# Kernel tuning notes

Hardware: AMD Instinct MI355X
Metric: run time of the kernel (lower is better)

The kernel has to match this reference:

```python
import jax, jax.numpy as jnp
import numpy as np

N, E, F_IN, H, K = 100000, 1600000, 256, 128, 5


def setup_inputs() -> dict:
    key = jax.random.key(0)
    ks = jax.random.split(key, 24)

    def rn(k, shape, scale=0.05):
        return jax.random.normal(k, shape, dtype=jnp.float32) * scale

    inp = {
        "x": rn(ks[0], (N, F_IN), 1.0),
        "edge_index": jax.random.randint(ks[1], (2, E), 0, N, dtype=jnp.int64),
        "edge_attr": jax.random.uniform(ks[2], (N, K), dtype=jnp.float32),
        "pre_W": rn(ks[3], (F_IN, H)),
        "pre_b": jnp.zeros((H,), jnp.float32),
        "c1_Ws": rn(ks[4], (H, H)),
        "c1_Wn": rn(ks[5], (H, H)),
        "c1_b": jnp.zeros((H,), jnp.float32),
        "c2_Ws": rn(ks[6], (H, H)),
        "c2_Wn": rn(ks[7], (H, H)),
        "c2_b": jnp.zeros((H,), jnp.float32),
        "nodepost_W": rn(ks[8], (H, H)),
        "nodepost_b": jnp.zeros((H,), jnp.float32),
        "d_W0": rn(ks[9], (K, H)),
        "d_b0": jnp.zeros((H,), jnp.float32),
        "d_W1": rn(ks[10], (H, H)),
        "d_b1": jnp.zeros((H,), jnp.float32),
        "d_W2": rn(ks[11], (H, H)),
        "d_b2": jnp.zeros((H,), jnp.float32),
        "d_W3": rn(ks[12], (H, H)),
        "d_b3": jnp.zeros((H,), jnp.float32),
        "final_W": rn(ks[13], (2 * H, 1)),
        "final_b": jnp.zeros((1,), jnp.float32),
    }
    return inp


def _mean_agg(h, src, dst, n):
    # scatter-mean of source features onto destination nodes
    s = jax.ops.segment_sum(h[src], dst, num_segments=n)  # [N, H]
    deg = jax.ops.segment_sum(jnp.ones_like(dst, dtype=h.dtype), dst, num_segments=n)
    return s / jnp.maximum(deg, 1.0)[:, None]


def reference(x, edge_index, edge_attr, pre_W, pre_b,
              c1_Ws, c1_Wn, c1_b, c2_Ws, c2_Wn, c2_b,
              nodepost_W, nodepost_b,
              d_W0, d_b0, d_W1, d_b1, d_W2, d_b2, d_W3, d_b3,
              final_W, final_b):
    n = x.shape[0]
    src, dst = edge_index[0], edge_index[1]

    # --- feat path: NodeAttributeAggregator ---
    h = x @ pre_W + pre_b                                   # pre_process_mlp
    agg = _mean_agg(h, src, dst, n)
    h = jax.nn.relu(h @ c1_Ws + agg @ c1_Wn + c1_b)          # layer1 conv + act
    agg = _mean_agg(h, src, dst, n)
    h = jax.nn.relu(h @ c2_Ws + agg @ c2_Wn + c2_b)          # layer2 conv + act
    feat_out = h @ nodepost_W + nodepost_b                   # post_process_mlp

    # --- dist path: EdgeAttributeAggregator (MLP over edge attrs) ---
    e = edge_attr.reshape(-1, K)
    y = jax.nn.relu(e @ d_W0 + d_b0)
    y = jax.nn.relu(y @ d_W1 + d_b1)
    y = jax.nn.relu(y @ d_W2 + d_b2)
    dist_out = y @ d_W3 + d_b3

    # --- merge 'cat' + final MLP + squeeze + sigmoid ---
    z = jnp.concatenate([feat_out, dist_out], axis=1)        # [N, 2H]
    out = (z @ final_W + final_b).squeeze(1)                  # [N]
    return jax.nn.sigmoid(out)
```

## Files before the change

### kernel.cpp

```cpp
#include <hip/hip_runtime.h>

#define HF 128
#define CAP 64
#define PSHIFT 17
#define BUCKET_BLOCKS 2048
#define BKS 68

typedef __attribute__((ext_vector_type(8))) short s16x8;
typedef __attribute__((ext_vector_type(4))) float f32x4;
typedef __attribute__((ext_vector_type(2))) float f32x2;

__device__ __forceinline__ unsigned short f2bf(float f) {
    unsigned u = __float_as_uint(f);
    return (unsigned short)((u + 0x7fff + ((u >> 16) & 1)) >> 16);
}

#if __has_builtin(__builtin_amdgcn_cvt_pk_fp8_f32) && __has_builtin(__builtin_amdgcn_cvt_pk_f32_fp8)
#define FP8_HW 1
#else
#define FP8_HW 0
#endif

__device__ __forceinline__ unsigned char f2fp8(float f) {
#if FP8_HW
    int v = __builtin_amdgcn_cvt_pk_fp8_f32(f, f, 0, false);
    return (unsigned char)(v & 0xff);
#else
    unsigned u = __float_as_uint(f);
    unsigned s = (u >> 24) & 0x80;
    float a = fabsf(f);
    if (a > 448.f) a = 448.f;
    if (a < 0.015625f) {
        int q = (int)(a * 512.f + 0.5f);
        return (unsigned char)(s | q);
    }
    unsigned ub = __float_as_uint(a);
    ub += 0x0007ffff + ((ub >> 20) & 1);
    int e8 = (int)(ub >> 23) - 127 + 7;
    if (e8 >= 16) return (unsigned char)(s | 0x7e);
    return (unsigned char)(s | (e8 << 3) | ((ub >> 20) & 7));
#endif
}

__device__ __forceinline__ void fp8acc4(unsigned w, float* acc) {
#if FP8_HW
    f32x2 lo = __builtin_amdgcn_cvt_pk_f32_fp8(w, false);
    f32x2 hi = __builtin_amdgcn_cvt_pk_f32_fp8(w, true);
    acc[0] += lo.x; acc[1] += lo.y; acc[2] += hi.x; acc[3] += hi.y;
#else
    #pragma unroll
    for (int j = 0; j < 4; ++j) {
        unsigned b = (w >> (8 * j)) & 0xff;
        unsigned s = (b >> 7) & 1, e = (b >> 3) & 15, m = b & 7;
        float v = e ? __uint_as_float(((e + 120) << 23) | (m << 20))
                    : (float)m * 0.001953125f;
        acc[j] += s ? -v : v;
    }
#endif
}

__device__ __forceinline__ void repack_one(
    const float* __restrict__ W, short* __restrict__ Wp, int K, int t)
{
    int nkt = K >> 5;
    int lane = t & 63;
    int kt = (t >> 6) % nkt;
    int nt = (t >> 6) / nkt;
    int c = nt * 16 + (lane & 15);
    int kbase = kt * 32 + (lane >> 4) * 8;
    s16x8 v;
    #pragma unroll
    for (int j = 0; j < 8; ++j) v[j] = (short)f2bf(W[(long)(kbase + j) * HF + c]);
    *(s16x8*)(Wp + (long)t * 8) = v;
}

__global__ __launch_bounds__(256) void repack_all(
    const float* __restrict__ preW, const float* __restrict__ c1Ws,
    const float* __restrict__ c1Wn, const float* __restrict__ c2Ws,
    const float* __restrict__ c2Wn, const float* __restrict__ dW1,
    const float* __restrict__ dW2,
    short* preWp, short* c1Wsp, short* c1Wnp, short* c2Wsp, short* c2Wnp,
    short* dW1p, short* dW2p,
    const float* __restrict__ npW, const float* __restrict__ npb,
    const float* __restrict__ dW3, const float* __restrict__ db3,
    const float* __restrict__ fW,  const float* __restrict__ fb,
    float* __restrict__ uvc)
{
    int b = blockIdx.x;
    if (b == 64) {
        int i = threadIdx.x;
        if (i < HF) {
            float u = 0.f, v = 0.f;
            for (int j = 0; j < HF; ++j) {
                u += npW[i * HF + j] * fW[j];
                v += dW3[i * HF + j] * fW[HF + j];
            }
            uvc[i] = u;
            uvc[HF + i] = v;
            if (i == 0) {
                float c = fb[0];
                for (int j = 0; j < HF; ++j) c += npb[j] * fW[j] + db3[j] * fW[HF + j];
                uvc[2 * HF] = c;
            }
        }
        return;
    }
    if (b < 16) { repack_one(preW, preWp, 256, b * 256 + threadIdx.x); return; }
    int m = (b - 16) >> 3, t = ((b - 16) & 7) * 256 + threadIdx.x;
    const float* W; short* Wp;
    switch (m) {
        case 0: W = c1Ws; Wp = c1Wsp; break;
        case 1: W = c1Wn; Wp = c1Wnp; break;
        case 2: W = c2Ws; Wp = c2Wsp; break;
        case 3: W = c2Wn; Wp = c2Wnp; break;
        case 4: W = dW1;  Wp = dW1p;  break;
        default: W = dW2; Wp = dW2p;  break;
    }
    repack_one(W, Wp, HF, t);
}

__global__ __launch_bounds__(256) void bucketx_kernel(
    const int* __restrict__ eidx, long E,
    int* __restrict__ deg, int* __restrict__ bucket, int npass)
{
    const int xcd   = blockIdx.x & 7;
    const int chunk = blockIdx.x >> 3;
    const int nchunks = BUCKET_BLOCKS / 8;
    long per = (E + nchunks - 1) / nchunks;
    per = (per + 3) & ~3L;
    const long e0 = (long)chunk * per;
    const long e1 = (e0 + per < E) ? e0 + per : E;
    if (e0 >= E) return;
    for (int p = 0; p < npass; ++p) {
        for (long e = e0 + (long)threadIdx.x * 4; e + 4 <= e1; e += 1024) {
            int4 d4 = *(const int4*)(eidx + E + e);
            #pragma unroll
            for (int j = 0; j < 4; ++j) {
                int d = (&d4.x)[j];
                if ((d >> PSHIFT) != p || ((d >> 4) & 7) != xcd) continue;
                int s = eidx[e + j];
                int pos = atomicAdd(&deg[d], 1);
                if (pos < CAP) bucket[(long)d * CAP + pos] = s;
            }
        }
        for (long e = (e1 & ~3L) + threadIdx.x; e < e1; e += 256) {
            int d = eidx[E + e];
            if ((d >> PSHIFT) != p || ((d >> 4) & 7) != xcd) continue;
            int s = eidx[e];
            int pos = atomicAdd(&deg[d], 1);
            if (pos < CAP) bucket[(long)d * CAP + pos] = s;
        }
    }
}

__device__ __forceinline__ void stage_bucket(
    const int* __restrict__ bucket, const int* __restrict__ deg,
    long row0B, int n, int* ldsbkt, int* ldsdeg)
{
    const uint4* gb = (const uint4*)(bucket + row0B * CAP);
    #pragma unroll
    for (int h = 0; h < 2; ++h) {
        int u = threadIdx.x + h * 512;
        int row = u >> 4, q = u & 15;
        *(uint4*)&ldsbkt[row * BKS + q * 4] = gb[u];
    }
    if (threadIdx.x < 64) {
        long node = row0B + threadIdx.x;
        ldsdeg[threadIdx.x] = (node < n) ? deg[node] : 0;
    }
}

__device__ __forceinline__ void agg_tile_v2(
    const unsigned char* __restrict__ hq,
    const int* ldsbkt, const int* ldsdeg,
    int n, long row0B, int wv, int lane, unsigned* ldsagg)
{
    const int r = lane >> 3;
    const int i = lane & 7;
    const int rg = wv * 8 + r;

    const int dg = ldsdeg[rg];
    const int m  = dg < CAP ? dg : CAP;
    int maxm = m;
    maxm = max(maxm, __shfl_xor(maxm, 8, 64));
    maxm = max(maxm, __shfl_xor(maxm, 16, 64));
    maxm = max(maxm, __shfl_xor(maxm, 32, 64));

    float acc[16];
    #pragma unroll
    for (int j = 0; j < 16; ++j) acc[j] = 0.f;

    const int* bl = ldsbkt + rg * BKS;
    for (int e = 0; e < maxm; e += 8) {
        int4 ia = *(const int4*)(bl + e);
        int4 ib = *(const int4*)(bl + e + 4);
        int s0 = (e + 0 < m) ? ia.x : 0;
        int s1 = (e + 1 < m) ? ia.y : 0;
        int s2 = (e + 2 < m) ? ia.z : 0;
        int s3 = (e + 3 < m) ? ia.w : 0;
        int s4 = (e + 4 < m) ? ib.x : 0;
        int s5 = (e + 5 < m) ? ib.y : 0;
        int s6 = (e + 6 < m) ? ib.z : 0;
        int s7 = (e + 7 < m) ? ib.w : 0;
        uint4 v0 = *(const uint4*)(hq + (long)s0 * HF + i * 16);
        uint4 v1 = *(const uint4*)(hq + (long)s1 * HF + i * 16);
        uint4 v2 = *(const uint4*)(hq + (long)s2 * HF + i * 16);
        uint4 v3 = *(const uint4*)(hq + (long)s3 * HF + i * 16);
        uint4 v4 = *(const uint4*)(hq + (long)s4 * HF + i * 16);
        uint4 v5 = *(const uint4*)(hq + (long)s5 * HF + i * 16);
        uint4 v6 = *(const uint4*)(hq + (long)s6 * HF + i * 16);
        uint4 v7 = *(const uint4*)(hq + (long)s7 * HF + i * 16);
        if (e + 0 < m) { fp8acc4(v0.x, acc); fp8acc4(v0.y, acc + 4); fp8acc4(v0.z, acc + 8); fp8acc4(v0.w, acc + 12); }
        if (e + 1 < m) { fp8acc4(v1.x, acc); fp8acc4(v1.y, acc + 4); fp8acc4(v1.z, acc + 8); fp8acc4(v1.w, acc + 12); }
        if (e + 2 < m) { fp8acc4(v2.x, acc); fp8acc4(v2.y, acc + 4); fp8acc4(v2.z, acc + 8); fp8acc4(v2.w, acc + 12); }
        if (e + 3 < m) { fp8acc4(v3.x, acc); fp8acc4(v3.y, acc + 4); fp8acc4(v3.z, acc + 8); fp8acc4(v3.w, acc + 12); }
        if (e + 4 < m) { fp8acc4(v4.x, acc); fp8acc4(v4.y, acc + 4); fp8acc4(v4.z, acc + 8); fp8acc4(v4.w, acc + 12); }
        if (e + 5 < m) { fp8acc4(v5.x, acc); fp8acc4(v5.y, acc + 4); fp8acc4(v5.z, acc + 8); fp8acc4(v5.w, acc + 12); }
        if (e + 6 < m) { fp8acc4(v6.x, acc); fp8acc4(v6.y, acc + 4); fp8acc4(v6.z, acc + 8); fp8acc4(v6.w, acc + 12); }
        if (e + 7 < m) { fp8acc4(v7.x, acc); fp8acc4(v7.y, acc + 4); fp8acc4(v7.z, acc + 8); fp8acc4(v7.w, acc + 12); }
    }

    const float sc = 1.f / (float)(dg > 1 ? dg : 1);
    unsigned pk[8];
    #pragma unroll
    for (int j = 0; j < 8; ++j)
        pk[j] = (unsigned)f2bf(acc[2 * j] * sc) | ((unsigned)f2bf(acc[2 * j + 1] * sc) << 16);
    const int c0 = 2 * i, c1 = 2 * i + 1, s = rg & 15;
    *(uint4*)&ldsagg[rg * 64 + ((c0 ^ s) << 2)] = make_uint4(pk[0], pk[1], pk[2], pk[3]);
    *(uint4*)&ldsagg[rg * 64 + ((c1 ^ s) << 2)] = make_uint4(pk[4], pk[5], pk[6], pk[7]);
}

__device__ __forceinline__ void gemm_pass4(
    const unsigned short* __restrict__ Av, const short* __restrict__ Wp,
    long rA, int lane, int nb, f32x4 acc[4])
{
    const int q = lane >> 4;
    #pragma unroll
    for (int kt = 0; kt < 4; ++kt) {
        s16x8 a = *(const s16x8*)(Av + rA * HF + kt * 32 + q * 8);
        #pragma unroll
        for (int j = 0; j < 4; ++j) {
            s16x8 b = *(const s16x8*)(Wp + ((long)((nb + j) * 4 + kt) * 64 + lane) * 8);
            acc[j] = __builtin_amdgcn_mfma_f32_16x16x32_bf16(a, b, acc[j], 0, 0, 0);
        }
    }
}

__device__ __forceinline__ void gemm_pass_lds4(
    const unsigned* lds, int w3, int lane, const short* __restrict__ Wp,
    int nb, f32x4 acc[4])
{
    const int q = lane >> 4;
    const int i15 = lane & 15;
    const int rl = w3 * 16 + i15;
    #pragma unroll
    for (int kt = 0; kt < 4; ++kt) {
        s16x8 a = *(const s16x8*)&lds[rl * 64 + (((kt * 4 + q) ^ i15) << 2)];
        #pragma unroll
        for (int j = 0; j < 4; ++j) {
            s16x8 b = *(const s16x8*)(Wp + ((long)((nb + j) * 4 + kt) * 64 + lane) * 8);
            acc[j] = __builtin_amdgcn_mfma_f32_16x16x32_bf16(a, b, acc[j], 0, 0, 0);
        }
    }
}

__device__ __forceinline__ void gemm_pass_mfma8(
    const unsigned short* __restrict__ Av, const short* __restrict__ Wp,
    long rA, int lane, f32x4 acc[8])
{
    const int q = lane >> 4;
    #pragma unroll
    for (int kt = 0; kt < 4; ++kt) {
        s16x8 a = *(const s16x8*)(Av + rA * HF + kt * 32 + q * 8);
        #pragma unroll
        for (int nt = 0; nt < 8; ++nt) {
            s16x8 b = *(const s16x8*)(Wp + ((long)(nt * 4 + kt) * 64 + lane) * 8);
            acc[nt] = __builtin_amdgcn_mfma_f32_16x16x32_bf16(a, b, acc[nt], 0, 0, 0);
        }
    }
}

__device__ __forceinline__ void gemm_pass_lds8(
    const unsigned* lds, int w3, int lane, const short* __restrict__ Wp, f32x4 acc[8])
{
    const int q = lane >> 4;
    const int i15 = lane & 15;
    const int rl = w3 * 16 + i15;
    #pragma unroll
    for (int kt = 0; kt < 4; ++kt) {
        s16x8 a = *(const s16x8*)&lds[rl * 64 + (((kt * 4 + q) ^ i15) << 2)];
        #pragma unroll
        for (int nt = 0; nt < 8; ++nt) {
            s16x8 b = *(const s16x8*)(Wp + ((long)(nt * 4 + kt) * 64 + lane) * 8);
            acc[nt] = __builtin_amdgcn_mfma_f32_16x16x32_bf16(a, b, acc[nt], 0, 0, 0);
        }
    }
}

__global__ __launch_bounds__(512) void prek_kernel(
    const float* __restrict__ x, const short* __restrict__ preWp,
    const float* __restrict__ preb, unsigned short* __restrict__ h0,
    unsigned char* __restrict__ h0q, int n)
{
    __shared__ float ldsx[64 * 256];
    const int lane = threadIdx.x & 63;
    const int wv   = threadIdx.x >> 6;
    const long row0B = (long)blockIdx.x * 64;

    #pragma unroll
    for (int rr = 0; rr < 8; ++rr) {
        const int row = wv * 8 + rr;
        const long gr = row0B + row;
        if (gr < n) {
            const int s = row & 7;
            const float* gp = x + gr * 256 + ((lane ^ s) << 2);
#if __has_builtin(__builtin_amdgcn_global_load_lds)
            __builtin_amdgcn_global_load_lds(
                (const __attribute__((address_space(1))) void*)gp,
                (__attribute__((address_space(3))) void*)&ldsx[row * 256], 16, 0, 0);
#else
            float4 f = *(const float4*)gp;
            *(float4*)&ldsx[row * 256 + lane * 4] = f;
#endif
        }
    }
    __syncthreads();

    const int w3 = wv & 3;
    const int nb = (wv >> 2) * 4;
    const int q  = lane >> 4;
    const int l15 = lane & 15;
    const int rl = w3 * 16 + l15;
    const int s  = rl & 7;

    f32x4 acc[4];
    #pragma unroll
    for (int j = 0; j < 4; ++j)
        #pragma unroll
        for (int i = 0; i < 4; ++i) acc[j][i] = 0.f;

    #pragma unroll
    for (int kt = 0; kt < 8; ++kt) {
        const int c0 = kt * 8 + q * 2;
        float4 f0 = *(const float4*)&ldsx[rl * 256 + ((c0 ^ s) << 2)];
        float4 f1 = *(const float4*)&ldsx[rl * 256 + (((c0 + 1) ^ s) << 2)];
        s16x8 a;
        a[0] = (short)f2bf(f0.x); a[1] = (short)f2bf(f0.y);
        a[2] = (short)f2bf(f0.z); a[3] = (short)f2bf(f0.w);
        a[4] = (short)f2bf(f1.x); a[5] = (short)f2bf(f1.y);
        a[6] = (short)f2bf(f1.z); a[7] = (short)f2bf(f1.w);
        #pragma unroll
        for (int j = 0; j < 4; ++j) {
            s16x8 b = *(const s16x8*)(preWp + ((long)((nb + j) * 8 + kt) * 64 + lane) * 8);
            acc[j] = __builtin_amdgcn_mfma_f32_16x16x32_bf16(a, b, acc[j], 0, 0, 0);
        }
    }
    __syncthreads();

    unsigned short* lp16 = (unsigned short*)ldsx;
    unsigned char*  lp8  = (unsigned char*)ldsx + 16384;
    const int cq = lane >> 4;
    #pragma unroll
    for (int j = 0; j < 4; ++j) {
        int col = (nb + j) * 16 + l15;
        float bs = preb[col];
        #pragma unroll
        for (int i = 0; i < 4; ++i) {
            int row = w3 * 16 + cq * 4 + i;
            float o = acc[j][i] + bs;
            lp16[row * 128 + col] = f2bf(o);
            lp8[row * 128 + col]  = f2fp8(o);
        }
    }
    __syncthreads();

    const int r = threadIdx.x >> 3;
    const int c = (threadIdx.x & 7) * 16;
    const long gr = row0B + r;
    if (gr < n) {
        uint4* src = (uint4*)&lp16[r * 128 + c];
        *(uint4*)(h0 + gr * HF + c)     = src[0];
        *(uint4*)(h0 + gr * HF + c + 8) = src[1];
        *(uint4*)(h0q + gr * HF + c)    = *(uint4*)&lp8[r * 128 + c];
    }
}

__global__ __launch_bounds__(512) void disthead_kernel(
    const float* __restrict__ ea, const float* __restrict__ W0,
    const float* __restrict__ b0, const short* __restrict__ W1p,
    const float* __restrict__ b1, unsigned short* __restrict__ y1, int n)
{
    __shared__ unsigned short lpk[64 * 128];
    const int lane = threadIdx.x & 63;
    const int wv   = threadIdx.x >> 6;
    const int w3   = wv & 3;
    const int nb   = (wv >> 2) * 4;
    const long row0B = (long)blockIdx.x * 64;
    const long row0 = row0B + w3 * 16;
    const int q = lane >> 4;
    long rA = row0 + (lane & 15);
    if (rA > n - 1) rA = n - 1;

    float e0 = ea[rA * 5 + 0], e1 = ea[rA * 5 + 1], e2 = ea[rA * 5 + 2],
          e3 = ea[rA * 5 + 3], e4 = ea[rA * 5 + 4];

    f32x4 acc[4];
    #pragma unroll
    for (int j = 0; j < 4; ++j)
        #pragma unroll
        for (int i = 0; i < 4; ++i) acc[j][i] = 0.f;

    #pragma unroll
    for (int kt = 0; kt < 4; ++kt) {
        const int c = kt * 32 + q * 8;
        s16x8 a;
        #pragma unroll
        for (int h = 0; h < 2; ++h) {
            float4 w0 = *(const float4*)(W0 + 0 * HF + c + h * 4);
            float4 w1 = *(const float4*)(W0 + 1 * HF + c + h * 4);
            float4 w2 = *(const float4*)(W0 + 2 * HF + c + h * 4);
            float4 w3v = *(const float4*)(W0 + 3 * HF + c + h * 4);
            float4 w4 = *(const float4*)(W0 + 4 * HF + c + h * 4);
            float4 bb = *(const float4*)(b0 + c + h * 4);
            float z0 = fmaxf(bb.x + e0 * w0.x + e1 * w1.x + e2 * w2.x + e3 * w3v.x + e4 * w4.x, 0.f);
            float z1 = fmaxf(bb.y + e0 * w0.y + e1 * w1.y + e2 * w2.y + e3 * w3v.y + e4 * w4.y, 0.f);
            float z2 = fmaxf(bb.z + e0 * w0.z + e1 * w1.z + e2 * w2.z + e3 * w3v.z + e4 * w4.z, 0.f);
            float z3 = fmaxf(bb.w + e0 * w0.w + e1 * w1.w + e2 * w2.w + e3 * w3v.w + e4 * w4.w, 0.f);
            a[h * 4 + 0] = (short)f2bf(z0); a[h * 4 + 1] = (short)f2bf(z1);
            a[h * 4 + 2] = (short)f2bf(z2); a[h * 4 + 3] = (short)f2bf(z3);
        }
        #pragma unroll
        for (int j = 0; j < 4; ++j) {
            s16x8 b = *(const s16x8*)(W1p + ((long)((nb + j) * 4 + kt) * 64 + lane) * 8);
            acc[j] = __builtin_amdgcn_mfma_f32_16x16x32_bf16(a, b, acc[j], 0, 0, 0);
        }
    }

    const int cq = lane >> 4;
    const int l15 = lane & 15;
    #pragma unroll
    for (int j = 0; j < 4; ++j) {
        int col = (nb + j) * 16 + l15;
        float bs = b1[col];
        #pragma unroll
        for (int i = 0; i < 4; ++i) {
            int row = w3 * 16 + cq * 4 + i;
            lpk[row * 128 + col] = f2bf(fmaxf(acc[j][i] + bs, 0.f));
        }
    }
    __syncthreads();

    const int r = threadIdx.x >> 3;
    const int c = (threadIdx.x & 7) * 16;
    const long gr = row0B + r;
    if (gr < n) {
        uint4* src = (uint4*)&lpk[r * 128 + c];
        *(uint4*)(y1 + gr * HF + c)     = src[0];
        *(uint4*)(y1 + gr * HF + c + 8) = src[1];
    }
}

__global__ __launch_bounds__(512) void c1f_kernel(
    const unsigned short* __restrict__ h0, const unsigned char* __restrict__ h0q,
    const int* __restrict__ deg, const int* __restrict__ bucket,
    const short* __restrict__ Wsp, const short* __restrict__ Wnp,
    const float* __restrict__ bias, unsigned short* __restrict__ out,
    unsigned char* __restrict__ outq, int n)
{
    __shared__ unsigned ldsagg[64 * 64];
    __shared__ int ldsbkt[64 * BKS];
    __shared__ int ldsdeg[64];
    const int lane = threadIdx.x & 63;
    const int wv   = threadIdx.x >> 6;
    const long row0B = (long)blockIdx.x * 64;

    stage_bucket(bucket, deg, row0B, n, ldsbkt, ldsdeg);
    __syncthreads();
    agg_tile_v2(h0q, ldsbkt, ldsdeg, n, row0B, wv, lane, ldsagg);
    __syncthreads();

    const int w3 = wv & 3;
    const int nb = (wv >> 2) * 4;

    f32x4 acc[4];
    #pragma unroll
    for (int j = 0; j < 4; ++j)
        #pragma unroll
        for (int i = 0; i < 4; ++i) acc[j][i] = 0.f;

    const long row0 = row0B + w3 * 16;
    long rA = row0 + (lane & 15);
    if (rA > n - 1) rA = n - 1;

    gemm_pass4(h0, Wsp, rA, lane, nb, acc);
    gemm_pass_lds4(ldsagg, w3, lane, Wnp, nb, acc);

    const int cq = lane >> 4;
    #pragma unroll
    for (int j = 0; j < 4; ++j) {
        int col = (nb + j) * 16 + (lane & 15);
        float bs = bias[col];
        #pragma unroll
        for (int i = 0; i < 4; ++i) {
            long r = row0 + cq * 4 + i;
            if (r < n) {
                float o = fmaxf(acc[j][i] + bs, 0.f);
                out[r * HF + col] = f2bf(o);
                outq[r * HF + col] = f2fp8(o);
            }
        }
    }
}

__global__ __launch_bounds__(512) void tailf_kernel(
    const unsigned short* __restrict__ h1, const unsigned char* __restrict__ h1q,
    const unsigned short* __restrict__ y1,
    const int* __restrict__ deg, const int* __restrict__ bucket,
    const short* __restrict__ c2Wsp, const short* __restrict__ c2Wnp,
    const short* __restrict__ dW2p,
    const float* __restrict__ c2b, const float* __restrict__ db2,
    const float* __restrict__ uvc, float* __restrict__ out, int n)
{
    __shared__ unsigned ldsagg[64 * 64];
    __shared__ int ldsbkt[64 * BKS];
    __shared__ int ldsdeg[64];
    __shared__ float pp[2][64];
    const int lane = threadIdx.x & 63;
    const int wv   = threadIdx.x >> 6;
    const long row0B = (long)blockIdx.x * 64;

    stage_bucket(bucket, deg, row0B, n, ldsbkt, ldsdeg);
    __syncthreads();
    agg_tile_v2(h1q, ldsbkt, ldsdeg, n, row0B, wv, lane, ldsagg);
    __syncthreads();

    const int w = wv & 3;
    const long row0 = row0B + w * 16;
    long rA = row0 + (lane & 15);
    if (rA > n - 1) rA = n - 1;
    const int cq = lane >> 4;
    float part[4] = {0.f, 0.f, 0.f, 0.f};

    f32x4 acc[8];
    #pragma unroll
    for (int nt = 0; nt < 8; ++nt)
        #pragma unroll
        for (int i = 0; i < 4; ++i) acc[nt][i] = 0.f;

    if (wv < 4) {
        gemm_pass_mfma8(h1, c2Wsp, rA, lane, acc);
        gemm_pass_lds8(ldsagg, w, lane, c2Wnp, acc);
        #pragma unroll
        for (int nt = 0; nt < 8; ++nt) {
            int col = nt * 16 + (lane & 15);
            float bh = c2b[col], uu = uvc[col];
            #pragma unroll
            for (int i = 0; i < 4; ++i)
                part[i] += fmaxf(acc[nt][i] + bh, 0.f) * uu;
        }
    } else {
        gemm_pass_mfma8(y1, dW2p, rA, lane, acc);
        #pragma unroll
        for (int nt = 0; nt < 8; ++nt) {
            int col = nt * 16 + (lane & 15);
            float by = db2[col], vv = uvc[HF + col];
            #pragma unroll
            for (int i = 0; i < 4; ++i)
                part[i] += fmaxf(acc[nt][i] + by, 0.f) * vv;
        }
    }

    #pragma unroll
    for (int i = 0; i < 4; ++i) {
        float s = part[i];
        s += __shfl_xor(s, 1, 64);
        s += __shfl_xor(s, 2, 64);
        s += __shfl_xor(s, 4, 64);
        s += __shfl_xor(s, 8, 64);
        part[i] = s;
    }
    if ((lane & 15) == 0) {
        #pragma unroll
        for (int i = 0; i < 4; ++i)
            pp[wv >> 2][w * 16 + cq * 4 + i] = part[i];
    }
    __syncthreads();

    if (threadIdx.x < 64) {
        long r = row0B + threadIdx.x;
        if (r < n) {
            float s = pp[0][threadIdx.x] + pp[1][threadIdx.x] + uvc[2 * HF];
            out[r] = 1.f / (1.f + expf(-s));
        }
    }
}

extern "C" void kernel_launch(void* const* d_in, const int* in_sizes, int n_in,
                              void* d_out, int out_size, void* d_ws, size_t ws_size,
                              hipStream_t stream)
{
    const float* x      = (const float*)d_in[0];
    const int*   eidx   = (const int*)  d_in[1];
    const float* eattr  = (const float*)d_in[2];
    const float* pre_W  = (const float*)d_in[3];
    const float* pre_b  = (const float*)d_in[4];
    const float* c1_Ws  = (const float*)d_in[5];
    const float* c1_Wn  = (const float*)d_in[6];
    const float* c1_b   = (const float*)d_in[7];
    const float* c2_Ws  = (const float*)d_in[8];
    const float* c2_Wn  = (const float*)d_in[9];
    const float* c2_b   = (const float*)d_in[10];
    const float* npW    = (const float*)d_in[11];
    const float* npb    = (const float*)d_in[12];
    const float* dW0    = (const float*)d_in[13];
    const float* db0    = (const float*)d_in[14];
    const float* dW1    = (const float*)d_in[15];
    const float* db1    = (const float*)d_in[16];
    const float* dW2    = (const float*)d_in[17];
    const float* db2    = (const float*)d_in[18];
    const float* dW3    = (const float*)d_in[19];
    const float* db3    = (const float*)d_in[20];
    const float* fW     = (const float*)d_in[21];
    const float* fb     = (const float*)d_in[22];

    const int  n = in_sizes[0] / 256;
    const long E = in_sizes[1] / 2;

    char* ws = (char*)d_ws;
    size_t off = 0;
    auto alloc = [&](size_t bytes) -> void* {
        void* p = ws + off;
        off += (bytes + 255) & ~(size_t)255;
        return p;
    };
    unsigned short* B0 = (unsigned short*)alloc((size_t)n * HF * 2);
    unsigned short* B1 = (unsigned short*)alloc((size_t)n * HF * 2);
    unsigned short* B2 = (unsigned short*)alloc((size_t)n * HF * 2);
    unsigned char*  B0q = (unsigned char*)alloc((size_t)n * HF);
    unsigned char*  B1q = (unsigned char*)alloc((size_t)n * HF);
    int*   deg    = (int*)alloc((size_t)n * sizeof(int));
    int*   bucket = (int*)alloc(((size_t)n + 64) * CAP * sizeof(int));
    float* uvc    = (float*)alloc((2 * HF + 1) * sizeof(float));
    short* preWp  = (short*)alloc(256 * HF * 2);
    short* c1Wsp  = (short*)alloc(HF * HF * 2);
    short* c1Wnp  = (short*)alloc(HF * HF * 2);
    short* c2Wsp  = (short*)alloc(HF * HF * 2);
    short* c2Wnp  = (short*)alloc(HF * HF * 2);
    short* dW1p   = (short*)alloc(HF * HF * 2);
    short* dW2p   = (short*)alloc(HF * HF * 2);

    const int gemmBlocks = (n + 63) / 64;
    const int npass = ((n - 1) >> PSHIFT) + 1;

    repack_all<<<65, 256, 0, stream>>>(
        pre_W, c1_Ws, c1_Wn, c2_Ws, c2_Wn, dW1, dW2,
        preWp, c1Wsp, c1Wnp, c2Wsp, c2Wnp, dW1p, dW2p,
        npW, npb, dW3, db3, fW, fb, uvc);

    hipMemsetAsync(deg, 0, (size_t)n * sizeof(int), stream);

    bucketx_kernel<<<BUCKET_BLOCKS, 256, 0, stream>>>(eidx, E, deg, bucket, npass);

    prek_kernel<<<gemmBlocks, 512, 0, stream>>>(x, preWp, pre_b, B0, B0q, n);

    disthead_kernel<<<gemmBlocks, 512, 0, stream>>>(
        eattr, dW0, db0, dW1p, db1, B2, n);

    c1f_kernel<<<gemmBlocks, 512, 0, stream>>>(
        B0, B0q, deg, bucket, c1Wsp, c1Wnp, c1_b, B1, B1q, n);

    tailf_kernel<<<gemmBlocks, 512, 0, stream>>>(
        B1, B1q, B2, deg, bucket, c2Wsp, c2Wnp, dW2p, c2_b, db2, uvc, (float*)d_out, n);
}
```

Baseline: 283.5 us.

## Replace atomic edge bucketing with a two-pass coarse-bin partition

Drops the single edge-bucketing kernel, which scanned the edge list once per XCD filter and did a global atomic per edge on the degree array. It is replaced by a two-kernel partition. The first kernel bins edges by destination range into coarse global bins, staging them in LDS and flushing in 8-entry chunks. The second kernel builds the per-node buckets and degrees for each bin using LDS atomics. The staging buffer reuses the B0 activation buffer before it is written. This adds an extra round trip of (src,dst) pairs through global memory, and edges are silently dropped if a bin overflows its capacity.

```diff
diff --git a/kernel.cpp b/kernel.cpp
--- a/kernel.cpp
+++ b/kernel.cpp
@@ -2,9 +2,9 @@
 
 #define HF 128
 #define CAP 64
-#define PSHIFT 17
-#define BUCKET_BLOCKS 2048
 #define BKS 68
+#define NBMAX 512
+#define SCAP1 8
 
 typedef __attribute__((ext_vector_type(8))) short s16x8;
 typedef __attribute__((ext_vector_type(4))) float f32x4;
@@ -119,37 +119,82 @@
     repack_one(W, Wp, HF, t);
 }
 
-__global__ __launch_bounds__(256) void bucketx_kernel(
-    const int* __restrict__ eidx, long E,
-    int* __restrict__ deg, int* __restrict__ bucket, int npass)
-{
-    const int xcd   = blockIdx.x & 7;
-    const int chunk = blockIdx.x >> 3;
-    const int nchunks = BUCKET_BLOCKS / 8;
-    long per = (E + nchunks - 1) / nchunks;
-    per = (per + 3) & ~3L;
-    const long e0 = (long)chunk * per;
+__global__ __launch_bounds__(256) void part1_kernel(
+    const int* __restrict__ eidx, long E, int nb, int sh,
+    int* __restrict__ gcount, uint2* __restrict__ binbuf, long bcap)
+{
+    __shared__ int scount[NBMAX];
+    __shared__ uint2 sbuf[NBMAX * SCAP1];
+    for (int i = threadIdx.x; i < nb; i += 256) scount[i] = 0;
+    __syncthreads();
+
+    const long per = (E + gridDim.x - 1) / gridDim.x;
+    const long e0 = (long)blockIdx.x * per;
     const long e1 = (e0 + per < E) ? e0 + per : E;
-    if (e0 >= E) return;
-    for (int p = 0; p < npass; ++p) {
-        for (long e = e0 + (long)threadIdx.x * 4; e + 4 <= e1; e += 1024) {
-            int4 d4 = *(const int4*)(eidx + E + e);
-            #pragma unroll
-            for (int j = 0; j < 4; ++j) {
-                int d = (&d4.x)[j];
-                if ((d >> PSHIFT) != p || ((d >> 4) & 7) != xcd) continue;
-                int s = eidx[e + j];
-                int pos = atomicAdd(&deg[d], 1);
-                if (pos < CAP) bucket[(long)d * CAP + pos] = s;
+
+    for (long base = e0; base < e1; base += 256) {
+        long e = base + threadIdx.x;
+        if (e < e1) {
+            int s = eidx[e];
+            int d = eidx[E + e];
+            int b = d >> sh;
+            int p = atomicAdd(&scount[b], 1);
+            if (p < SCAP1) {
+                sbuf[b * SCAP1 + p] = make_uint2((unsigned)s, (unsigned)d);
+            } else {
+                int g = atomicAdd(&gcount[b], 1);
+                if (g < bcap) binbuf[(long)b * bcap + g] = make_uint2((unsigned)s, (unsigned)d);
             }
         }
-        for (long e = (e1 & ~3L) + threadIdx.x; e < e1; e += 256) {
-            int d = eidx[E + e];
-            if ((d >> PSHIFT) != p || ((d >> 4) & 7) != xcd) continue;
-            int s = eidx[e];
-            int pos = atomicAdd(&deg[d], 1);
-            if (pos < CAP) bucket[(long)d * CAP + pos] = s;
-        }
+        __syncthreads();
+        for (int b = threadIdx.x; b < nb; b += 256) {
+            int c = scount[b]; if (c > SCAP1) c = SCAP1;
+            if (c == SCAP1) {
+                int g = atomicAdd(&gcount[b], SCAP1);
+                if (g + SCAP1 <= bcap) {
+                    uint4* dst = (uint4*)(binbuf + (long)b * bcap + g);
+                    const uint4* src = (const uint4*)(sbuf + b * SCAP1);
+                    dst[0] = src[0]; dst[1] = src[1];
+                    dst[2] = src[2]; dst[3] = src[3];
+                }
+                scount[b] = 0;
+            } else {
+                scount[b] = c;
+            }
+        }
+        __syncthreads();
+    }
+    for (int b = threadIdx.x; b < nb; b += 256) {
+        int c = scount[b]; if (c > SCAP1) c = SCAP1;
+        if (c > 0) {
+            int g = atomicAdd(&gcount[b], c);
+            for (int j = 0; j < c; ++j)
+                if (g + j < bcap) binbuf[(long)b * bcap + g + j] = sbuf[b * SCAP1 + j];
+        }
+    }
+}
+
+__global__ __launch_bounds__(256) void part2_kernel(
+    const uint2* __restrict__ binbuf, const int* __restrict__ gcount, long bcap,
+    int sh, int* __restrict__ deg, int* __restrict__ bucket, int n)
+{
+    __shared__ int cur[NBMAX];
+    const int b = blockIdx.x;
+    const int base = b << sh;
+    const int range = 1 << sh;
+    for (int i = threadIdx.x; i < range; i += 256) cur[i] = 0;
+    __syncthreads();
+    int cnt = gcount[b]; if (cnt > (int)bcap) cnt = (int)bcap;
+    const uint2* src = binbuf + (long)b * bcap;
+    for (int i = threadIdx.x; i < cnt; i += 256) {
+        uint2 sd = src[i];
+        int pos = atomicAdd(&cur[(int)sd.y - base], 1);
+        if (pos < CAP) bucket[(long)sd.y * CAP + pos] = (int)sd.x;
+    }
+    __syncthreads();
+    for (int i = threadIdx.x; i < range; i += 256) {
+        int node = base + i;
+        if (node < n) deg[node] = cur[i];
     }
 }
 
@@ -648,18 +693,28 @@
     short* c2Wnp  = (short*)alloc(HF * HF * 2);
     short* dW1p   = (short*)alloc(HF * HF * 2);
     short* dW2p   = (short*)alloc(HF * HF * 2);
+    int*   gcount = (int*)alloc(NBMAX * sizeof(int));
+
+    int sh = 8;
+    while ((((long)(n - 1) >> sh) + 1) > NBMAX) ++sh;
+    const int nb = (int)(((long)(n - 1) >> sh) + 1);
+    long bcap = ((E / nb) * 9) / 8 + 64;
+    bcap = (bcap + 7) & ~7L;
+    long maxcap = ((long)n * 256) / ((long)nb * 8);
+    if (bcap > maxcap) bcap = maxcap & ~7L;
+    uint2* binbuf = (uint2*)B0;
 
     const int gemmBlocks = (n + 63) / 64;
-    const int npass = ((n - 1) >> PSHIFT) + 1;
 
     repack_all<<<65, 256, 0, stream>>>(
         pre_W, c1_Ws, c1_Wn, c2_Ws, c2_Wn, dW1, dW2,
         preWp, c1Wsp, c1Wnp, c2Wsp, c2Wnp, dW1p, dW2p,
         npW, npb, dW3, db3, fW, fb, uvc);
 
-    hipMemsetAsync(deg, 0, (size_t)n * sizeof(int), stream);
-
-    bucketx_kernel<<<BUCKET_BLOCKS, 256, 0, stream>>>(eidx, E, deg, bucket, npass);
+    hipMemsetAsync(gcount, 0, NBMAX * sizeof(int), stream);
+
+    part1_kernel<<<512, 256, 0, stream>>>(eidx, E, nb, sh, gcount, binbuf, bcap);
+    part2_kernel<<<nb, 256, 0, stream>>>(binbuf, gcount, bcap, sh, deg, bucket, n);
 
     prek_kernel<<<gemmBlocks, 512, 0, stream>>>(x, preWp, pre_b, B0, B0q, n);
 
```

Result: slower. 315.7 us (+11.3%).

## Merge edge bucketing and distance-head MLP into one interleaved launch

Applied to the files above, without the earlier changes.

Replaces the separate bucketing and distance-head kernels with a single launch whose blocks are proportionally split between the two jobs. The atomic-bound edge bucketing can then overlap with the MFMA-based edge-attribute MLP, and one launch gap disappears. The distance head is rewritten for 256 threads: each wave covers all 8 column tiles and writes bf16 results straight to global memory, with no LDS staging. Two risks come with this. The bucket chunk's XCD index now comes from a logical block number rather than the hardware block index, so the atomic-locality mapping may no longer line up. The direct scalar stores are also less coalesced.

```diff
diff --git a/kernel.cpp b/kernel.cpp
--- a/kernel.cpp
+++ b/kernel.cpp
@@ -119,12 +119,12 @@
     repack_one(W, Wp, HF, t);
 }
 
-__global__ __launch_bounds__(256) void bucketx_kernel(
-    const int* __restrict__ eidx, long E,
+__device__ void bucket_body(
+    int bb, const int* __restrict__ eidx, long E,
     int* __restrict__ deg, int* __restrict__ bucket, int npass)
 {
-    const int xcd   = blockIdx.x & 7;
-    const int chunk = blockIdx.x >> 3;
+    const int xcd   = bb & 7;
+    const int chunk = bb >> 3;
     const int nchunks = BUCKET_BLOCKS / 8;
     long per = (E + nchunks - 1) / nchunks;
     per = (per + 3) & ~3L;
@@ -150,6 +150,84 @@
             int pos = atomicAdd(&deg[d], 1);
             if (pos < CAP) bucket[(long)d * CAP + pos] = s;
         }
+    }
+}
+
+__device__ void disthead_body(int gb,
+    const float* __restrict__ ea, const float* __restrict__ W0,
+    const float* __restrict__ b0, const short* __restrict__ W1p,
+    const float* __restrict__ b1, unsigned short* __restrict__ y1, int n)
+{
+    const int lane = threadIdx.x & 63;
+    const int wv   = threadIdx.x >> 6;
+    const long row0 = (long)gb * 64 + wv * 16;
+    const int q = lane >> 4;
+    long rA = row0 + (lane & 15);
+    if (rA > n - 1) rA = n - 1;
+
+    float e0 = ea[rA * 5 + 0], e1 = ea[rA * 5 + 1], e2 = ea[rA * 5 + 2],
+          e3 = ea[rA * 5 + 3], e4 = ea[rA * 5 + 4];
+
+    f32x4 acc[8];
+    #pragma unroll
+    for (int nt = 0; nt < 8; ++nt)
+        #pragma unroll
+        for (int i = 0; i < 4; ++i) acc[nt][i] = 0.f;
+
+    #pragma unroll
+    for (int kt = 0; kt < 4; ++kt) {
+        const int c = kt * 32 + q * 8;
+        s16x8 a;
+        #pragma unroll
+        for (int h = 0; h < 2; ++h) {
+            float4 w0 = *(const float4*)(W0 + 0 * HF + c + h * 4);
+            float4 w1 = *(const float4*)(W0 + 1 * HF + c + h * 4);
+            float4 w2 = *(const float4*)(W0 + 2 * HF + c + h * 4);
+            float4 w3v = *(const float4*)(W0 + 3 * HF + c + h * 4);
+            float4 w4 = *(const float4*)(W0 + 4 * HF + c + h * 4);
+            float4 bb = *(const float4*)(b0 + c + h * 4);
+            float z0 = fmaxf(bb.x + e0 * w0.x + e1 * w1.x + e2 * w2.x + e3 * w3v.x + e4 * w4.x, 0.f);
+            float z1 = fmaxf(bb.y + e0 * w0.y + e1 * w1.y + e2 * w2.y + e3 * w3v.y + e4 * w4.y, 0.f);
+            float z2 = fmaxf(bb.z + e0 * w0.z + e1 * w1.z + e2 * w2.z + e3 * w3v.z + e4 * w4.z, 0.f);
+            float z3 = fmaxf(bb.w + e0 * w0.w + e1 * w1.w + e2 * w2.w + e3 * w3v.w + e4 * w4.w, 0.f);
+            a[h * 4 + 0] = (short)f2bf(z0); a[h * 4 + 1] = (short)f2bf(z1);
+            a[h * 4 + 2] = (short)f2bf(z2); a[h * 4 + 3] = (short)f2bf(z3);
+        }
+        #pragma unroll
+        for (int nt = 0; nt < 8; ++nt) {
+            s16x8 b = *(const s16x8*)(W1p + ((long)(nt * 4 + kt) * 64 + lane) * 8);
+            acc[nt] = __builtin_amdgcn_mfma_f32_16x16x32_bf16(a, b, acc[nt], 0, 0, 0);
+        }
+    }
+
+    const int cq = lane >> 4;
+    #pragma unroll
+    for (int nt = 0; nt < 8; ++nt) {
+        int col = nt * 16 + (lane & 15);
+        float bs = b1[col];
+        #pragma unroll
+        for (int i = 0; i < 4; ++i) {
+            long r = row0 + cq * 4 + i;
+            if (r < n) y1[r * HF + col] = f2bf(fmaxf(acc[nt][i] + bs, 0.f));
+        }
+    }
+}
+
+__global__ __launch_bounds__(256) void megabd_kernel(
+    const int* __restrict__ eidx, long E,
+    int* __restrict__ deg, int* __restrict__ bucket, int npass,
+    const float* __restrict__ ea, const float* __restrict__ W0,
+    const float* __restrict__ b0, const short* __restrict__ W1p,
+    const float* __restrict__ b1, unsigned short* __restrict__ y1,
+    int n, int total)
+{
+    const long bid = blockIdx.x;
+    const long bcnt0 = (bid * BUCKET_BLOCKS) / total;
+    const long bcnt1 = ((bid + 1) * BUCKET_BLOCKS) / total;
+    if (bcnt1 > bcnt0) {
+        bucket_body((int)bcnt0, eidx, E, deg, bucket, npass);
+    } else {
+        disthead_body((int)(bid - bcnt1), ea, W0, b0, W1p, b1, y1, n);
     }
 }
 
@@ -385,81 +463,6 @@
     }
 }
 
-__global__ __launch_bounds__(512) void disthead_kernel(
-    const float* __restrict__ ea, const float* __restrict__ W0,
-    const float* __restrict__ b0, const short* __restrict__ W1p,
-    const float* __restrict__ b1, unsigned short* __restrict__ y1, int n)
-{
-    __shared__ unsigned short lpk[64 * 128];
-    const int lane = threadIdx.x & 63;
-    const int wv   = threadIdx.x >> 6;
-    const int w3   = wv & 3;
-    const int nb   = (wv >> 2) * 4;
-    const long row0B = (long)blockIdx.x * 64;
-    const long row0 = row0B + w3 * 16;
-    const int q = lane >> 4;
-    long rA = row0 + (lane & 15);
-    if (rA > n - 1) rA = n - 1;
-
-    float e0 = ea[rA * 5 + 0], e1 = ea[rA * 5 + 1], e2 = ea[rA * 5 + 2],
-          e3 = ea[rA * 5 + 3], e4 = ea[rA * 5 + 4];
-
-    f32x4 acc[4];
-    #pragma unroll
-    for (int j = 0; j < 4; ++j)
-        #pragma unroll
-        for (int i = 0; i < 4; ++i) acc[j][i] = 0.f;
-
-    #pragma unroll
-    for (int kt = 0; kt < 4; ++kt) {
-        const int c = kt * 32 + q * 8;
-        s16x8 a;
-        #pragma unroll
-        for (int h = 0; h < 2; ++h) {
-            float4 w0 = *(const float4*)(W0 + 0 * HF + c + h * 4);
-            float4 w1 = *(const float4*)(W0 + 1 * HF + c + h * 4);
-            float4 w2 = *(const float4*)(W0 + 2 * HF + c + h * 4);
-            float4 w3v = *(const float4*)(W0 + 3 * HF + c + h * 4);
-            float4 w4 = *(const float4*)(W0 + 4 * HF + c + h * 4);
-            float4 bb = *(const float4*)(b0 + c + h * 4);
-            float z0 = fmaxf(bb.x + e0 * w0.x + e1 * w1.x + e2 * w2.x + e3 * w3v.x + e4 * w4.x, 0.f);
-            float z1 = fmaxf(bb.y + e0 * w0.y + e1 * w1.y + e2 * w2.y + e3 * w3v.y + e4 * w4.y, 0.f);
-            float z2 = fmaxf(bb.z + e0 * w0.z + e1 * w1.z + e2 * w2.z + e3 * w3v.z + e4 * w4.z, 0.f);
-            float z3 = fmaxf(bb.w + e0 * w0.w + e1 * w1.w + e2 * w2.w + e3 * w3v.w + e4 * w4.w, 0.f);
-            a[h * 4 + 0] = (short)f2bf(z0); a[h * 4 + 1] = (short)f2bf(z1);
-            a[h * 4 + 2] = (short)f2bf(z2); a[h * 4 + 3] = (short)f2bf(z3);
-        }
-        #pragma unroll
-        for (int j = 0; j < 4; ++j) {
-            s16x8 b = *(const s16x8*)(W1p + ((long)((nb + j) * 4 + kt) * 64 + lane) * 8);
-            acc[j] = __builtin_amdgcn_mfma_f32_16x16x32_bf16(a, b, acc[j], 0, 0, 0);
-        }
-    }
-
-    const int cq = lane >> 4;
-    const int l15 = lane & 15;
-    #pragma unroll
-    for (int j = 0; j < 4; ++j) {
-        int col = (nb + j) * 16 + l15;
-        float bs = b1[col];
-        #pragma unroll
-        for (int i = 0; i < 4; ++i) {
-            int row = w3 * 16 + cq * 4 + i;
-            lpk[row * 128 + col] = f2bf(fmaxf(acc[j][i] + bs, 0.f));
-        }
-    }
-    __syncthreads();
-
-    const int r = threadIdx.x >> 3;
-    const int c = (threadIdx.x & 7) * 16;
-    const long gr = row0B + r;
-    if (gr < n) {
-        uint4* src = (uint4*)&lpk[r * 128 + c];
-        *(uint4*)(y1 + gr * HF + c)     = src[0];
-        *(uint4*)(y1 + gr * HF + c + 8) = src[1];
-    }
-}
-
 __global__ __launch_bounds__(512) void c1f_kernel(
     const unsigned short* __restrict__ h0, const unsigned char* __restrict__ h0q,
     const int* __restrict__ deg, const int* __restrict__ bucket,
@@ -659,12 +662,13 @@
 
     hipMemsetAsync(deg, 0, (size_t)n * sizeof(int), stream);
 
-    bucketx_kernel<<<BUCKET_BLOCKS, 256, 0, stream>>>(eidx, E, deg, bucket, npass);
+    const int total = BUCKET_BLOCKS + gemmBlocks;
+    megabd_kernel<<<total, 256, 0, stream>>>(
+        eidx, E, deg, bucket, npass,
+        eattr, dW0, db0, dW1p, db1, B2,
+        n, total);
 
     prek_kernel<<<gemmBlocks, 512, 0, stream>>>(x, preWp, pre_b, B0, B0q, n);
-
-    disthead_kernel<<<gemmBlocks, 512, 0, stream>>>(
-        eattr, dW0, db0, dW1p, db1, B2, n);
 
     c1f_kernel<<<gemmBlocks, 512, 0, stream>>>(
         B0, B0q, deg, bucket, c1Wsp, c1Wnp, c1_b, B1, B1q, n);
```

Measured after the change: 272.7 us. -3.8%, faster.

## Fuse dist-head MLP into pre-process kernel and skip unused bucket slots

Applied to the files above, without the earlier changes.

Merges the separate disthead kernel into the pre-process GEMM kernel, so the edge-attribute MLP runs while the x tile loads into LDS. This removes one launch and overlaps the dist-head compute with the x load latency. The bucket staging now copies only the slots a node actually uses, based on its degree, which cuts global reads for low-degree nodes. The fused kernel needs more registers to hold the packed dist outputs, which may lower occupancy.

```diff
diff --git a/kernel.cpp b/kernel.cpp
--- a/kernel.cpp
+++ b/kernel.cpp
@@ -157,16 +157,20 @@
     const int* __restrict__ bucket, const int* __restrict__ deg,
     long row0B, int n, int* ldsbkt, int* ldsdeg)
 {
+    if (threadIdx.x < 64) {
+        long node = row0B + threadIdx.x;
+        ldsdeg[threadIdx.x] = (node < n) ? deg[node] : 0;
+    }
     const uint4* gb = (const uint4*)(bucket + row0B * CAP);
     #pragma unroll
     for (int h = 0; h < 2; ++h) {
         int u = threadIdx.x + h * 512;
         int row = u >> 4, q = u & 15;
-        *(uint4*)&ldsbkt[row * BKS + q * 4] = gb[u];
-    }
-    if (threadIdx.x < 64) {
-        long node = row0B + threadIdx.x;
-        ldsdeg[threadIdx.x] = (node < n) ? deg[node] : 0;
+        long node = row0B + row;
+        int dgr = (node < n) ? deg[node] : 0;
+        if (dgr > CAP) dgr = CAP;
+        if (q * 4 < dgr)
+            *(uint4*)&ldsbkt[row * BKS + q * 4] = gb[u];
     }
 }
 
@@ -297,15 +301,23 @@
     }
 }
 
-__global__ __launch_bounds__(512) void prek_kernel(
+__global__ __launch_bounds__(512) void prekd_kernel(
     const float* __restrict__ x, const short* __restrict__ preWp,
     const float* __restrict__ preb, unsigned short* __restrict__ h0,
-    unsigned char* __restrict__ h0q, int n)
+    unsigned char* __restrict__ h0q,
+    const float* __restrict__ ea, const float* __restrict__ W0,
+    const float* __restrict__ b0, const short* __restrict__ W1p,
+    const float* __restrict__ b1, unsigned short* __restrict__ y1, int n)
 {
     __shared__ float ldsx[64 * 256];
     const int lane = threadIdx.x & 63;
     const int wv   = threadIdx.x >> 6;
     const long row0B = (long)blockIdx.x * 64;
+    const int w3 = wv & 3;
+    const int nb = (wv >> 2) * 4;
+    const int q  = lane >> 4;
+    const int l15 = lane & 15;
+    const int cq = lane >> 4;
 
     #pragma unroll
     for (int rr = 0; rr < 8; ++rr) {
@@ -324,15 +336,60 @@
 #endif
         }
     }
-    __syncthreads();
-
-    const int w3 = wv & 3;
-    const int nb = (wv >> 2) * 4;
-    const int q  = lane >> 4;
-    const int l15 = lane & 15;
+
+    unsigned py[8];
+    {
+        long rA = row0B + w3 * 16 + l15;
+        if (rA > n - 1) rA = n - 1;
+        float e0 = ea[rA * 5 + 0], e1 = ea[rA * 5 + 1], e2 = ea[rA * 5 + 2],
+              e3 = ea[rA * 5 + 3], e4 = ea[rA * 5 + 4];
+
+        f32x4 accd[4];
+        #pragma unroll
+        for (int j = 0; j < 4; ++j)
+            #pragma unroll
+            for (int i = 0; i < 4; ++i) accd[j][i] = 0.f;
+
+        #pragma unroll
+        for (int kt = 0; kt < 4; ++kt) {
+            const int c = kt * 32 + q * 8;
+            s16x8 a;
+            #pragma unroll
+            for (int h = 0; h < 2; ++h) {
+                float4 w0 = *(const float4*)(W0 + 0 * HF + c + h * 4);
+                float4 w1 = *(const float4*)(W0 + 1 * HF + c + h * 4);
+                float4 w2 = *(const float4*)(W0 + 2 * HF + c + h * 4);
+                float4 w3v = *(const float4*)(W0 + 3 * HF + c + h * 4);
+                float4 w4 = *(const float4*)(W0 + 4 * HF + c + h * 4);
+                float4 bb = *(const float4*)(b0 + c + h * 4);
+                float z0 = fmaxf(bb.x + e0 * w0.x + e1 * w1.x + e2 * w2.x + e3 * w3v.x + e4 * w4.x, 0.f);
+                float z1 = fmaxf(bb.y + e0 * w0.y + e1 * w1.y + e2 * w2.y + e3 * w3v.y + e4 * w4.y, 0.f);
+                float z2 = fmaxf(bb.z + e0 * w0.z + e1 * w1.z + e2 * w2.z + e3 * w3v.z + e4 * w4.z, 0.f);
+                float z3 = fmaxf(bb.w + e0 * w0.w + e1 * w1.w + e2 * w2.w + e3 * w3v.w + e4 * w4.w, 0.f);
+                a[h * 4 + 0] = (short)f2bf(z0); a[h * 4 + 1] = (short)f2bf(z1);
+                a[h * 4 + 2] = (short)f2bf(z2); a[h * 4 + 3] = (short)f2bf(z3);
+            }
+            #pragma unroll
+            for (int j = 0; j < 4; ++j) {
+                s16x8 b = *(const s16x8*)(W1p + ((long)((nb + j) * 4 + kt) * 64 + lane) * 8);
+                accd[j] = __builtin_amdgcn_mfma_f32_16x16x32_bf16(a, b, accd[j], 0, 0, 0);
+            }
+        }
+        #pragma unroll
+        for (int j = 0; j < 4; ++j) {
+            float bs = b1[(nb + j) * 16 + l15];
+            unsigned short v0 = f2bf(fmaxf(accd[j][0] + bs, 0.f));
+            unsigned short v1 = f2bf(fmaxf(accd[j][1] + bs, 0.f));
+            unsigned short v2 = f2bf(fmaxf(accd[j][2] + bs, 0.f));
+            unsigned short v3 = f2bf(fmaxf(accd[j][3] + bs, 0.f));
+            py[j * 2]     = (unsigned)v0 | ((unsigned)v1 << 16);
+            py[j * 2 + 1] = (unsigned)v2 | ((unsigned)v3 << 16);
+        }
+    }
+    __syncthreads();
+
     const int rl = w3 * 16 + l15;
     const int s  = rl & 7;
-
     f32x4 acc[4];
     #pragma unroll
     for (int j = 0; j < 4; ++j)
@@ -357,9 +414,9 @@
     }
     __syncthreads();
 
-    unsigned short* lp16 = (unsigned short*)ldsx;
-    unsigned char*  lp8  = (unsigned char*)ldsx + 16384;
-    const int cq = lane >> 4;
+    unsigned short* lp16  = (unsigned short*)ldsx;
+    unsigned char*  lp8   = (unsigned char*)ldsx + 16384;
+    unsigned short* lp16y = (unsigned short*)((char*)ldsx + 24576);
     #pragma unroll
     for (int j = 0; j < 4; ++j) {
         int col = (nb + j) * 16 + l15;
@@ -370,6 +427,7 @@
             float o = acc[j][i] + bs;
             lp16[row * 128 + col] = f2bf(o);
             lp8[row * 128 + col]  = f2fp8(o);
+            lp16y[row * 128 + col] = (unsigned short)(py[j * 2 + (i >> 1)] >> ((i & 1) * 16));
         }
     }
     __syncthreads();
@@ -378,85 +436,13 @@
     const int c = (threadIdx.x & 7) * 16;
     const long gr = row0B + r;
     if (gr < n) {
-        uint4* src = (uint4*)&lp16[r * 128 + c];
-        *(uint4*)(h0 + gr * HF + c)     = src[0];
-        *(uint4*)(h0 + gr * HF + c + 8) = src[1];
+        uint4* s16p = (uint4*)&lp16[r * 128 + c];
+        *(uint4*)(h0 + gr * HF + c)     = s16p[0];
+        *(uint4*)(h0 + gr * HF + c + 8) = s16p[1];
         *(uint4*)(h0q + gr * HF + c)    = *(uint4*)&lp8[r * 128 + c];
-    }
-}
-
-__global__ __launch_bounds__(512) void disthead_kernel(
-    const float* __restrict__ ea, const float* __restrict__ W0,
-    const float* __restrict__ b0, const short* __restrict__ W1p,
-    const float* __restrict__ b1, unsigned short* __restrict__ y1, int n)
-{
-    __shared__ unsigned short lpk[64 * 128];
-    const int lane = threadIdx.x & 63;
-    const int wv   = threadIdx.x >> 6;
-    const int w3   = wv & 3;
-    const int nb   = (wv >> 2) * 4;
-    const long row0B = (long)blockIdx.x * 64;
-    const long row0 = row0B + w3 * 16;
-    const int q = lane >> 4;
-    long rA = row0 + (lane & 15);
-    if (rA > n - 1) rA = n - 1;
-
-    float e0 = ea[rA * 5 + 0], e1 = ea[rA * 5 + 1], e2 = ea[rA * 5 + 2],
-          e3 = ea[rA * 5 + 3], e4 = ea[rA * 5 + 4];
-
-    f32x4 acc[4];
-    #pragma unroll
-    for (int j = 0; j < 4; ++j)
-        #pragma unroll
-        for (int i = 0; i < 4; ++i) acc[j][i] = 0.f;
-
-    #pragma unroll
-    for (int kt = 0; kt < 4; ++kt) {
-        const int c = kt * 32 + q * 8;
-        s16x8 a;
-        #pragma unroll
-        for (int h = 0; h < 2; ++h) {
-            float4 w0 = *(const float4*)(W0 + 0 * HF + c + h * 4);
-            float4 w1 = *(const float4*)(W0 + 1 * HF + c + h * 4);
-            float4 w2 = *(const float4*)(W0 + 2 * HF + c + h * 4);
-            float4 w3v = *(const float4*)(W0 + 3 * HF + c + h * 4);
-            float4 w4 = *(const float4*)(W0 + 4 * HF + c + h * 4);
-            float4 bb = *(const float4*)(b0 + c + h * 4);
-            float z0 = fmaxf(bb.x + e0 * w0.x + e1 * w1.x + e2 * w2.x + e3 * w3v.x + e4 * w4.x, 0.f);
-            float z1 = fmaxf(bb.y + e0 * w0.y + e1 * w1.y + e2 * w2.y + e3 * w3v.y + e4 * w4.y, 0.f);
-            float z2 = fmaxf(bb.z + e0 * w0.z + e1 * w1.z + e2 * w2.z + e3 * w3v.z + e4 * w4.z, 0.f);
-            float z3 = fmaxf(bb.w + e0 * w0.w + e1 * w1.w + e2 * w2.w + e3 * w3v.w + e4 * w4.w, 0.f);
-            a[h * 4 + 0] = (short)f2bf(z0); a[h * 4 + 1] = (short)f2bf(z1);
-            a[h * 4 + 2] = (short)f2bf(z2); a[h * 4 + 3] = (short)f2bf(z3);
-        }
-        #pragma unroll
-        for (int j = 0; j < 4; ++j) {
-            s16x8 b = *(const s16x8*)(W1p + ((long)((nb + j) * 4 + kt) * 64 + lane) * 8);
-            acc[j] = __builtin_amdgcn_mfma_f32_16x16x32_bf16(a, b, acc[j], 0, 0, 0);
-        }
-    }
-
-    const int cq = lane >> 4;
-    const int l15 = lane & 15;
-    #pragma unroll
-    for (int j = 0; j < 4; ++j) {
-        int col = (nb + j) * 16 + l15;
-        float bs = b1[col];
-        #pragma unroll
-        for (int i = 0; i < 4; ++i) {
-            int row = w3 * 16 + cq * 4 + i;
-            lpk[row * 128 + col] = f2bf(fmaxf(acc[j][i] + bs, 0.f));
-        }
-    }
-    __syncthreads();
-
-    const int r = threadIdx.x >> 3;
-    const int c = (threadIdx.x & 7) * 16;
-    const long gr = row0B + r;
-    if (gr < n) {
-        uint4* src = (uint4*)&lpk[r * 128 + c];
-        *(uint4*)(y1 + gr * HF + c)     = src[0];
-        *(uint4*)(y1 + gr * HF + c + 8) = src[1];
+        uint4* sy = (uint4*)&lp16y[r * 128 + c];
+        *(uint4*)(y1 + gr * HF + c)     = sy[0];
+        *(uint4*)(y1 + gr * HF + c + 8) = sy[1];
     }
 }
 
@@ -661,9 +647,8 @@
 
     bucketx_kernel<<<BUCKET_BLOCKS, 256, 0, stream>>>(eidx, E, deg, bucket, npass);
 
-    prek_kernel<<<gemmBlocks, 512, 0, stream>>>(x, preWp, pre_b, B0, B0q, n);
-
-    disthead_kernel<<<gemmBlocks, 512, 0, stream>>>(
+    prekd_kernel<<<gemmBlocks, 512, 0, stream>>>(
+        x, preWp, pre_b, B0, B0q,
         eattr, dW0, db0, dW1p, db1, B2, n);
 
     c1f_kernel<<<gemmBlocks, 512, 0, stream>>>(
```

New measurement: 282.8 us. Within noise of the previous version (-0.3%).
